# Optimization experiments

Hardware: AMD Instinct MI355X
Metric: run time of the kernel (lower is better)

Reference implementation:

```python
import jax, jax.numpy as jnp
import numpy as np

EMBED_DIM = 2048
NUM_HEADS = 16
NUM_GROUPS = 4
HEAD_DIM = EMBED_DIM // NUM_HEADS  # 128
B, S = 2, 2048


def setup_inputs() -> dict:
    key = jax.random.key(0)
    ks = jax.random.split(key, 7)
    sc = 0.02
    return {
        "x": jax.random.normal(ks[0], (B, S, EMBED_DIM), dtype=jnp.float32),
        "Wq": jax.random.normal(ks[1], (EMBED_DIM, EMBED_DIM), dtype=jnp.float32) * sc,
        "bq": jnp.zeros((EMBED_DIM,), dtype=jnp.float32),
        "Wkv": jax.random.normal(ks[2], (EMBED_DIM, 2 * EMBED_DIM // NUM_GROUPS), dtype=jnp.float32) * sc,
        "bkv": jnp.zeros((2 * EMBED_DIM // NUM_GROUPS,), dtype=jnp.float32),
        "Wo": jax.random.normal(ks[3], (EMBED_DIM, EMBED_DIM), dtype=jnp.float32) * sc,
        "bo": jnp.zeros((EMBED_DIM,), dtype=jnp.float32),
    }


def reference(x, Wq, bq, Wkv, bkv, Wo, bo):
    b, s, e = x.shape
    group_size = NUM_HEADS // NUM_GROUPS
    # projections (torch Linear: x @ W + b with W stored [in, out] here)
    q = (x @ Wq + bq).reshape(b, s, NUM_HEADS, HEAD_DIM).transpose(0, 2, 1, 3)   # [B,H,S,D]
    kv = (x @ Wkv + bkv).reshape(b, s, NUM_GROUPS, 2 * HEAD_DIM).transpose(0, 2, 1, 3)  # [B,G,S,2D]
    k, v = kv[..., :HEAD_DIM], kv[..., HEAD_DIM:]                                # [B,G,S,D]
    # repeat each kv group for its heads (matches repeat_interleave on head dim)
    k = jnp.repeat(k, group_size, axis=1)                                        # [B,H,S,D]
    v = jnp.repeat(v, group_size, axis=1)                                        # [B,H,S,D]
    scores = jnp.einsum("bhqd,bhkd->bhqk", q, k) / (HEAD_DIM ** 0.5)             # [B,H,S,S]
    attn = jax.nn.softmax(scores, axis=-1)
    out = jnp.einsum("bhqk,bhkd->bhqd", attn, v)                                 # [B,H,S,D]
    out = out.transpose(0, 2, 1, 3).reshape(b, s, e)
    return out @ Wo + bo
```

## Files before the change

kernel.cpp:

```cpp
#include <hip/hip_runtime.h>

#define DEV __device__ __forceinline__

typedef unsigned short u16;
typedef unsigned int u32;
using bf16x8 = __attribute__((ext_vector_type(8))) __bf16;
using f32x4v = __attribute__((ext_vector_type(4))) float;

typedef __attribute__((address_space(1))) void gas_void;
typedef __attribute__((address_space(3))) void las_void;

DEV u16 f32_bf16(float f){
  u32 u = __float_as_uint(f);
  u += 0x7FFFu + ((u >> 16) & 1u);
  return (u16)(u >> 16);
}
DEV float bf16_f32(u16 h){ return __uint_as_float(((u32)h) << 16); }

DEV void gload16(const void* g, void* l){
  __builtin_amdgcn_global_load_lds((gas_void*)g, (las_void*)l, 16, 0, 0);
}

DEV float exp2_hw(float x){
  float r;
  asm("v_exp_f32 %0, %1" : "=v"(r) : "v"(x));
  return r;
}

#define QSCL 0.12752333f

__global__ void cvt_f32_bf16_k(const float* __restrict__ in, u16* __restrict__ out, int n){
  int i = (blockIdx.x * 256 + threadIdx.x) * 8;
  if (i >= n) return;
  float4 a = *(const float4*)(in + i);
  float4 b = *(const float4*)(in + i + 4);
  uint4 r;
  r.x = (u32)f32_bf16(a.x) | ((u32)f32_bf16(a.y) << 16);
  r.y = (u32)f32_bf16(a.z) | ((u32)f32_bf16(a.w) << 16);
  r.z = (u32)f32_bf16(b.x) | ((u32)f32_bf16(b.y) << 16);
  r.w = (u32)f32_bf16(b.z) | ((u32)f32_bf16(b.w) << 16);
  *(uint4*)(out + i) = r;
}

template<typename T>
__global__ void transpose_cvt_k(const T* __restrict__ in, u16* __restrict__ out, int R, int C){
  in  += (size_t)blockIdx.z * R * C;
  out += (size_t)blockIdx.z * R * C;
  __shared__ float tile[64][65];
  int c0 = blockIdx.x * 64, r0 = blockIdx.y * 64;
  int t = threadIdx.x;
  int lr = t >> 4;
  int lc = (t & 15) * 4;
  #pragma unroll
  for (int p = 0; p < 4; p++){
    int row = p * 16 + lr;
    const T* src = in + (size_t)(r0 + row) * C + c0 + lc;
    float v0, v1, v2, v3;
    if constexpr (sizeof(T) == 4){
      float4 v = *(const float4*)src;
      v0 = v.x; v1 = v.y; v2 = v.z; v3 = v.w;
    } else {
      ushort4 v = *(const ushort4*)src;
      v0 = bf16_f32(v.x); v1 = bf16_f32(v.y); v2 = bf16_f32(v.z); v3 = bf16_f32(v.w);
    }
    tile[row][lc+0] = v0; tile[row][lc+1] = v1; tile[row][lc+2] = v2; tile[row][lc+3] = v3;
  }
  __syncthreads();
  #pragma unroll
  for (int p = 0; p < 4; p++){
    int ocol = p * 16 + lr;
    ushort4 w;
    w.x = f32_bf16(tile[lc+0][ocol]);
    w.y = f32_bf16(tile[lc+1][ocol]);
    w.z = f32_bf16(tile[lc+2][ocol]);
    w.w = f32_bf16(tile[lc+3][ocol]);
    *(ushort4*)(out + (size_t)(c0 + ocol) * R + r0 + lc) = w;
  }
}

__global__ __launch_bounds__(512, 2)
void gemm256_k(const u16* __restrict__ A, const u16* __restrict__ BT,
               const float* __restrict__ bias0, const float* __restrict__ bias1,
               u16* __restrict__ outQ, u16* __restrict__ outK, u16* __restrict__ outV,
               float* __restrict__ outF, int K, int mode)
{
  __shared__ __align__(16) u16 sA[4][256*32];
  __shared__ __align__(16) u16 sB[4][256*32];
  const int t = threadIdx.x;
  const int l = t & 63, wv = t >> 6;
  const int wm = wv >> 2, wn = wv & 3;
  const int rl = l & 15, gr = l >> 4;
  const size_t m0 = (size_t)blockIdx.x * 256, n0 = (size_t)blockIdx.y * 256;
  const u16* gA = A + m0 * K;
  const u16* gB = BT + n0 * K;

  const u16* gAs[2]; const u16* gBs[2]; int ldso[2];
  #pragma unroll
  for (int j = 0; j < 2; j++){
    int c = t + j * 512;
    int row = c >> 2, cl = c & 3;
    int clp = cl ^ ((row >> 1) & 3);
    gAs[j] = gA + (size_t)row * K + clp * 8;
    gBs[j] = gB + (size_t)row * K + clp * 8;
    ldso[j] = c * 8;
  }
  auto stage = [&](int kt){
    int buf = kt & 3;
    int k0 = kt * 32;
    #pragma unroll
    for (int j = 0; j < 2; j++){
      gload16(gAs[j] + k0, &sA[buf][ldso[j]]);
      gload16(gBs[j] + k0, &sB[buf][ldso[j]]);
    }
  };

  const int swz8 = (gr ^ ((rl >> 1) & 3)) * 8;
  int offA[8], offB[4];
  #pragma unroll
  for (int mr = 0; mr < 8; mr++) offA[mr] = (wm*128 + mr*16 + rl) * 32 + swz8;
  #pragma unroll
  for (int nr = 0; nr < 4; nr++) offB[nr] = (wn*64 + nr*16 + rl) * 32 + swz8;

  f32x4v acc[8][4];
  #pragma unroll
  for (int i = 0; i < 8; i++)
    #pragma unroll
    for (int j = 0; j < 4; j++)
      acc[i][j] = (f32x4v)(0.0f);

  const int NT = K / 32;
  stage(0); stage(1);
  asm volatile("s_waitcnt vmcnt(4)" ::: "memory");
  __builtin_amdgcn_s_barrier();

  for (int kt = 0; kt < NT; kt++){
    const u16* sa = sA[kt & 3];
    const u16* sb = sB[kt & 3];
    bf16x8 af[8], bfr[4];
    #pragma unroll
    for (int mr = 0; mr < 8; mr++) af[mr] = *(const bf16x8*)(sa + offA[mr]);
    #pragma unroll
    for (int nr = 0; nr < 4; nr++) bfr[nr] = *(const bf16x8*)(sb + offB[nr]);
    if (kt + 2 < NT){
      stage(kt + 2);
      asm volatile("s_waitcnt vmcnt(4)" ::: "memory");
    } else {
      asm volatile("s_waitcnt vmcnt(0)" ::: "memory");
    }
    __builtin_amdgcn_s_barrier();
    __builtin_amdgcn_s_setprio(1);
    #pragma unroll
    for (int mr = 0; mr < 8; mr++)
      #pragma unroll
      for (int nr = 0; nr < 4; nr++)
        acc[mr][nr] = __builtin_amdgcn_mfma_f32_16x16x32_bf16(af[mr], bfr[nr], acc[mr][nr], 0, 0, 0);
    __builtin_amdgcn_s_setprio(0);
  }

  #pragma unroll
  for (int nr = 0; nr < 4; nr++){
    int col = (int)n0 + wn*64 + nr*16 + rl;
    float bv = (mode == 2 || col < 2048) ? bias0[col < 2048 ? col : 0] : 0.0f;
    if (mode != 2 && col >= 2048) bv = bias1[col - 2048];
    #pragma unroll
    for (int mr = 0; mr < 8; mr++){
      int rowb = (int)m0 + wm*128 + mr*16 + gr*4;
      #pragma unroll
      for (int r = 0; r < 4; r++){
        int row = rowb + r;
        float v = acc[mr][nr][r] + bv;
        if (mode == 2){
          outF[(size_t)row * 2048 + col] = v;
        } else if (col < 2048){
          int b = row >> 11, s = row & 2047, h = col >> 7, d = col & 127;
          outQ[(((size_t)(b*16 + h)) * 2048 + s) * 128 + d] = f32_bf16(v * QSCL);
        } else {
          int b = row >> 11, s = row & 2047;
          int c2 = col - 2048, g = c2 >> 8, cc = c2 & 255;
          u16* dst = (cc < 128) ? outK : outV;
          dst[(((size_t)(b*4 + g)) * 2048 + s) * 128 + (cc & 127)] = f32_bf16(v);
        }
      }
    }
  }
}

__global__ __launch_bounds__(256, 2)
void attn_k(const u16* __restrict__ Q, const u16* __restrict__ Kb,
            const u16* __restrict__ VT, u16* __restrict__ O)
{
  __shared__ __align__(16) u16 sK[2][64*128];
  __shared__ __align__(16) u16 sV[2][128*64];
  __shared__ __align__(16) u16 Plds[4][16*72];
  const int t = threadIdx.x, l = t & 63, wv = t >> 6;
  const int rl = l & 15, gr = l >> 4;
  const int bh = blockIdx.y;
  const int b = bh >> 4, h = bh & 15, g = h >> 2;
  const int q0 = blockIdx.x * 64 + wv * 16;
  const u16* Qp = Q + ((size_t)(b*16 + h) * 2048 + q0) * 128;
  const u16* Kp = Kb + (size_t)(b*4 + g) * 2048 * 128;
  const u16* Vp = VT + (size_t)(b*4 + g) * 128 * 2048;

  bf16x8 qf[4];
  #pragma unroll
  for (int ds = 0; ds < 4; ds++)
    qf[ds] = *(const bf16x8*)(Qp + rl*128 + ds*32 + gr*8);

  f32x4v acc_o[8];
  #pragma unroll
  for (int i = 0; i < 8; i++) acc_o[i] = (f32x4v)(0.0f);
  float m_run = -3.0e38f, l_run = 0.0f;

  auto stageKV = [&](int buf, int kt){
    const int kv0 = kt * 64;
    const u16* Ksrc = Kp + (size_t)kv0 * 128;
    #pragma unroll
    for (int j = 0; j < 4; j++){
      int n16 = j * 256 + t;
      int row = n16 >> 4, cl = n16 & 15;
      int sc = cl ^ (row & 7);
      gload16(Ksrc + row * 128 + sc * 8, &sK[buf][n16 * 8]);
    }
    const u16* Vsrc = Vp + kv0;
    #pragma unroll
    for (int j = 0; j < 4; j++){
      int n16 = j * 256 + t;
      int row = n16 >> 3, cl = n16 & 7;
      int sc = cl ^ (row & 7);
      gload16(Vsrc + (size_t)row * 2048 + sc * 8, &sV[buf][n16 * 8]);
    }
  };

  stageKV(0, 0);
  asm volatile("s_waitcnt vmcnt(0)" ::: "memory");
  __syncthreads();

  for (int kt = 0; kt < 32; kt++){
    const int cur = kt & 1;
    if (kt + 1 < 32) stageKV(cur ^ 1, kt + 1);
    const u16* sk = sK[cur];
    const u16* sv = sV[cur];

    float pv[4][4];
    float tm = -3.0e38f;
    #pragma unroll
    for (int tt = 0; tt < 4; tt++){
      f32x4v st = (f32x4v)(0.0f);
      bf16x8 kf[4];
      #pragma unroll
      for (int ds = 0; ds < 4; ds++){
        int r = tt*16 + rl;
        int c = ds*4 + gr;
        kf[ds] = *(const bf16x8*)(sk + r*128 + ((c ^ (r & 7)) * 8));
      }
      __builtin_amdgcn_s_setprio(1);
      #pragma unroll
      for (int ds = 0; ds < 4; ds++)
        st = __builtin_amdgcn_mfma_f32_16x16x32_bf16(kf[ds], qf[ds], st, 0, 0, 0);
      __builtin_amdgcn_s_setprio(0);
      #pragma unroll
      for (int r = 0; r < 4; r++){
        pv[tt][r] = st[r];
        tm = fmaxf(tm, st[r]);
      }
    }
    tm = fmaxf(tm, __shfl_xor(tm, 16, 64));
    tm = fmaxf(tm, __shfl_xor(tm, 32, 64));
    if (!__all(tm <= m_run + 11.0f)){
      float m_new = fmaxf(m_run, tm);
      float corr = exp2_hw(m_run - m_new);
      l_run *= corr;
      float cr0 = __shfl(corr, gr*4 + 0, 64);
      float cr1 = __shfl(corr, gr*4 + 1, 64);
      float cr2 = __shfl(corr, gr*4 + 2, 64);
      float cr3 = __shfl(corr, gr*4 + 3, 64);
      #pragma unroll
      for (int dc = 0; dc < 8; dc++){
        acc_o[dc][0] *= cr0; acc_o[dc][1] *= cr1; acc_o[dc][2] *= cr2; acc_o[dc][3] *= cr3;
      }
      m_run = m_new;
    }
    float psum = 0.f;
    #pragma unroll
    for (int tt = 0; tt < 4; tt++)
      #pragma unroll
      for (int r = 0; r < 4; r++){
        float p = exp2_hw(pv[tt][r] - m_run);
        pv[tt][r] = p;
        psum += p;
      }
    psum += __shfl_xor(psum, 16, 64);
    psum += __shfl_xor(psum, 32, 64);
    l_run += psum;

    #pragma unroll
    for (int tt = 0; tt < 4; tt++){
      ushort4 pk;
      pk.x = f32_bf16(pv[tt][0]); pk.y = f32_bf16(pv[tt][1]);
      pk.z = f32_bf16(pv[tt][2]); pk.w = f32_bf16(pv[tt][3]);
      *(ushort4*)&Plds[wv][rl*72 + tt*16 + gr*4] = pk;
    }
    asm volatile("s_waitcnt lgkmcnt(0)" ::: "memory");
    #pragma unroll
    for (int kc = 0; kc < 2; kc++){
      bf16x8 pa = *(const bf16x8*)&Plds[wv][rl*72 + kc*32 + gr*8];
      bf16x8 vf[8];
      #pragma unroll
      for (int dc = 0; dc < 8; dc++){
        int r = dc*16 + rl;
        int c = kc*4 + gr;
        vf[dc] = *(const bf16x8*)(sv + r*64 + ((c ^ (r & 7)) * 8));
      }
      __builtin_amdgcn_s_setprio(1);
      #pragma unroll
      for (int dc = 0; dc < 8; dc++)
        acc_o[dc] = __builtin_amdgcn_mfma_f32_16x16x32_bf16(pa, vf[dc], acc_o[dc], 0, 0, 0);
      __builtin_amdgcn_s_setprio(0);
    }
    asm volatile("s_waitcnt vmcnt(0)" ::: "memory");
    __syncthreads();
  }
  float linv = 1.0f / l_run;
  float lr0 = __shfl(linv, gr*4 + 0, 64);
  float lr1 = __shfl(linv, gr*4 + 1, 64);
  float lr2 = __shfl(linv, gr*4 + 2, 64);
  float lr3 = __shfl(linv, gr*4 + 3, 64);
  float lrr[4] = {lr0, lr1, lr2, lr3};
  #pragma unroll
  for (int dc = 0; dc < 8; dc++)
    #pragma unroll
    for (int r = 0; r < 4; r++){
      size_t idx = ((size_t)b * 2048 + q0 + gr*4 + r) * 2048 + h*128 + dc*16 + rl;
      O[idx] = f32_bf16(acc_o[dc][r] * lrr[r]);
    }
}

extern "C" void kernel_launch(void* const* d_in, const int* in_sizes, int n_in,
                              void* d_out, int out_size, void* d_ws, size_t ws_size,
                              hipStream_t stream)
{
  const float* x   = (const float*)d_in[0];
  const float* Wq  = (const float*)d_in[1];
  const float* bq  = (const float*)d_in[2];
  const float* Wkv = (const float*)d_in[3];
  const float* bkv = (const float*)d_in[4];
  const float* Wo  = (const float*)d_in[5];
  const float* bo  = (const float*)d_in[6];
  float* out = (float*)d_out;

  char* ws = (char*)d_ws;
  size_t off = 0;
  auto alloc = [&](size_t bytes){ void* p = ws + off; off = (off + bytes + 255) & ~(size_t)255; return p; };
  u16* xb     = (u16*)alloc(8388608ull * 2);
  u16* WqkvT  = (u16*)alloc(6291456ull * 2);
  u16* WoT    = (u16*)alloc(4194304ull * 2);
  u16* Qb     = (u16*)alloc(8388608ull * 2);
  u16* Kb     = (u16*)alloc(2097152ull * 2);
  u16* Vb     = (u16*)alloc(2097152ull * 2);
  u16* VTb    = (u16*)alloc(2097152ull * 2);
  u16* Ob     = (u16*)alloc(8388608ull * 2);

  cvt_f32_bf16_k<<<4096, 256, 0, stream>>>(x, xb, 8388608);
  transpose_cvt_k<float><<<dim3(32, 32, 1), 256, 0, stream>>>(Wq,  WqkvT, 2048, 2048);
  transpose_cvt_k<float><<<dim3(16, 32, 1), 256, 0, stream>>>(Wkv, WqkvT + 2048ull*2048ull, 2048, 1024);
  transpose_cvt_k<float><<<dim3(32, 32, 1), 256, 0, stream>>>(Wo,  WoT, 2048, 2048);

  gemm256_k<<<dim3(16, 12), 512, 0, stream>>>(xb, WqkvT, bq, bkv, Qb, Kb, Vb, nullptr, 2048, 0);

  transpose_cvt_k<u16><<<dim3(2, 32, 8), 256, 0, stream>>>(Vb, VTb, 2048, 128);

  attn_k<<<dim3(32, 32), 256, 0, stream>>>(Qb, Kb, VTb, Ob);

  gemm256_k<<<dim3(16, 8), 512, 0, stream>>>(Ob, WoT, bo, nullptr, nullptr, nullptr, nullptr, out, 2048, 2);
}
```

Baseline: 354.2 us.

## Use 32x32 MFMA attention with register P, fuse V transpose, narrow output GEMM

The attention kernel moves from 16x16x32 to 32x32x16 MFMA with 32 query rows per wave and 128 per block. The softmax probabilities are repacked in registers via cvt_pk and a lane-swap shuffle instead of a round trip through LDS. The QKV GEMM epilogue now writes V already transposed, which removes the separate transpose kernel and the Vb buffer. The output projection gets its own 256x128-tile GEMM so it launches 256 blocks instead of 128 for better CU fill. The trade-off is higher register pressure in attention and half as many attention blocks (512 instead of 1024).

```diff
diff --git a/kernel.cpp b/kernel.cpp
--- a/kernel.cpp
+++ b/kernel.cpp
@@ -6,6 +6,7 @@
 typedef unsigned int u32;
 using bf16x8 = __attribute__((ext_vector_type(8))) __bf16;
 using f32x4v = __attribute__((ext_vector_type(4))) float;
+using f32x16 = __attribute__((ext_vector_type(16))) float;
 
 typedef __attribute__((address_space(1))) void gas_void;
 typedef __attribute__((address_space(3))) void las_void;
@@ -25,6 +26,16 @@
   float r;
   asm("v_exp_f32 %0, %1" : "=v"(r) : "v"(x));
   return r;
+}
+DEV u32 cvtpk_bf16(float lo, float hi){
+  u32 r;
+  asm("v_cvt_pk_bf16_f32 %0, %1, %2" : "=v"(r) : "v"(lo), "v"(hi));
+  return r;
+}
+DEV bf16x8 mk_bf16x8(u32 a, u32 b, u32 c, u32 d){
+  union { u32 w[4]; bf16x8 v; } u;
+  u.w[0] = a; u.w[1] = b; u.w[2] = c; u.w[3] = d;
+  return u.v;
 }
 
 #define QSCL 0.12752333f
@@ -81,8 +92,8 @@
 __global__ __launch_bounds__(512, 2)
 void gemm256_k(const u16* __restrict__ A, const u16* __restrict__ BT,
                const float* __restrict__ bias0, const float* __restrict__ bias1,
-               u16* __restrict__ outQ, u16* __restrict__ outK, u16* __restrict__ outV,
-               float* __restrict__ outF, int K, int mode)
+               u16* __restrict__ outQ, u16* __restrict__ outK, u16* __restrict__ outVT,
+               int K)
 {
   __shared__ __align__(16) u16 sA[4][256*32];
   __shared__ __align__(16) u16 sB[4][256*32];
@@ -160,27 +171,127 @@
   #pragma unroll
   for (int nr = 0; nr < 4; nr++){
     int col = (int)n0 + wn*64 + nr*16 + rl;
-    float bv = (mode == 2 || col < 2048) ? bias0[col < 2048 ? col : 0] : 0.0f;
-    if (mode != 2 && col >= 2048) bv = bias1[col - 2048];
+    float bv = (col < 2048) ? bias0[col] : bias1[col - 2048];
     #pragma unroll
     for (int mr = 0; mr < 8; mr++){
       int rowb = (int)m0 + wm*128 + mr*16 + gr*4;
-      #pragma unroll
-      for (int r = 0; r < 4; r++){
-        int row = rowb + r;
-        float v = acc[mr][nr][r] + bv;
-        if (mode == 2){
-          outF[(size_t)row * 2048 + col] = v;
-        } else if (col < 2048){
-          int b = row >> 11, s = row & 2047, h = col >> 7, d = col & 127;
-          outQ[(((size_t)(b*16 + h)) * 2048 + s) * 128 + d] = f32_bf16(v * QSCL);
+      int b = rowb >> 11, s0 = rowb & 2047;
+      if (col < 2048){
+        int h = col >> 7, d = col & 127;
+        #pragma unroll
+        for (int r = 0; r < 4; r++)
+          outQ[(((size_t)(b*16 + h)) * 2048 + s0 + r) * 128 + d] =
+            f32_bf16((acc[mr][nr][r] + bv) * QSCL);
+      } else {
+        int c2 = col - 2048, g = c2 >> 8, cc = c2 & 255;
+        if (cc < 128){
+          #pragma unroll
+          for (int r = 0; r < 4; r++)
+            outK[(((size_t)(b*4 + g)) * 2048 + s0 + r) * 128 + cc] =
+              f32_bf16(acc[mr][nr][r] + bv);
         } else {
-          int b = row >> 11, s = row & 2047;
-          int c2 = col - 2048, g = c2 >> 8, cc = c2 & 255;
-          u16* dst = (cc < 128) ? outK : outV;
-          dst[(((size_t)(b*4 + g)) * 2048 + s) * 128 + (cc & 127)] = f32_bf16(v);
+          int d = cc - 128;
+          ushort4 w;
+          w.x = f32_bf16(acc[mr][nr][0] + bv);
+          w.y = f32_bf16(acc[mr][nr][1] + bv);
+          w.z = f32_bf16(acc[mr][nr][2] + bv);
+          w.w = f32_bf16(acc[mr][nr][3] + bv);
+          *(ushort4*)&outVT[(((size_t)(b*4 + g)) * 128 + d) * 2048 + s0] = w;
         }
       }
+    }
+  }
+}
+
+__global__ __launch_bounds__(512, 2)
+void gemm_o_k(const u16* __restrict__ A, const u16* __restrict__ BT,
+              const float* __restrict__ bias, float* __restrict__ outF, int K)
+{
+  __shared__ __align__(16) u16 sA[4][256*32];
+  __shared__ __align__(16) u16 sB[4][128*32];
+  const int t = threadIdx.x;
+  const int l = t & 63, wv = t >> 6;
+  const int wm = wv >> 2, wn = wv & 3;
+  const int rl = l & 15, gr = l >> 4;
+  const size_t m0 = (size_t)blockIdx.x * 256, n0 = (size_t)blockIdx.y * 128;
+  const u16* gA = A + m0 * K;
+  const u16* gB = BT + n0 * K;
+
+  const u16* gAs[2]; int ldsoA[2];
+  #pragma unroll
+  for (int j = 0; j < 2; j++){
+    int c = t + j * 512;
+    int row = c >> 2, cl = c & 3;
+    int clp = cl ^ ((row >> 1) & 3);
+    gAs[j] = gA + (size_t)row * K + clp * 8;
+    ldsoA[j] = c * 8;
+  }
+  const int rowB = t >> 2;
+  const int clB = (t & 3) ^ ((rowB >> 1) & 3);
+  const u16* gBs = gB + (size_t)rowB * K + clB * 8;
+  const int ldsoB = t * 8;
+
+  auto stage = [&](int kt){
+    int buf = kt & 3;
+    int k0 = kt * 32;
+    gload16(gAs[0] + k0, &sA[buf][ldsoA[0]]);
+    gload16(gAs[1] + k0, &sA[buf][ldsoA[1]]);
+    gload16(gBs + k0, &sB[buf][ldsoB]);
+  };
+
+  const int swz8 = (gr ^ ((rl >> 1) & 3)) * 8;
+  int offA[8], offB[2];
+  #pragma unroll
+  for (int mr = 0; mr < 8; mr++) offA[mr] = (wm*128 + mr*16 + rl) * 32 + swz8;
+  #pragma unroll
+  for (int nr = 0; nr < 2; nr++) offB[nr] = (wn*32 + nr*16 + rl) * 32 + swz8;
+
+  f32x4v acc[8][2];
+  #pragma unroll
+  for (int i = 0; i < 8; i++)
+    #pragma unroll
+    for (int j = 0; j < 2; j++)
+      acc[i][j] = (f32x4v)(0.0f);
+
+  const int NT = K / 32;
+  stage(0); stage(1);
+  asm volatile("s_waitcnt vmcnt(3)" ::: "memory");
+  __builtin_amdgcn_s_barrier();
+
+  for (int kt = 0; kt < NT; kt++){
+    const u16* sa = sA[kt & 3];
+    const u16* sb = sB[kt & 3];
+    bf16x8 af[8], bfr[2];
+    #pragma unroll
+    for (int mr = 0; mr < 8; mr++) af[mr] = *(const bf16x8*)(sa + offA[mr]);
+    #pragma unroll
+    for (int nr = 0; nr < 2; nr++) bfr[nr] = *(const bf16x8*)(sb + offB[nr]);
+    if (kt + 2 < NT){
+      stage(kt + 2);
+      asm volatile("s_waitcnt vmcnt(3)" ::: "memory");
+    } else {
+      asm volatile("s_waitcnt vmcnt(0)" ::: "memory");
+    }
+    __builtin_amdgcn_s_barrier();
+    __builtin_amdgcn_s_setprio(1);
+    #pragma unroll
+    for (int mr = 0; mr < 8; mr++)
+      #pragma unroll
+      for (int nr = 0; nr < 2; nr++)
+        acc[mr][nr] = __builtin_amdgcn_mfma_f32_16x16x32_bf16(af[mr], bfr[nr], acc[mr][nr], 0, 0, 0);
+    __builtin_amdgcn_s_setprio(0);
+  }
+
+  #pragma unroll
+  for (int nr = 0; nr < 2; nr++){
+    int col = (int)n0 + wn*32 + nr*16 + rl;
+    float bv = bias[col];
+    #pragma unroll
+    for (int mr = 0; mr < 8; mr++){
+      int rowb = (int)m0 + wm*128 + mr*16 + gr*4;
+      #pragma unroll
+      for (int r = 0; r < 4; r++)
+        outF[(size_t)(rowb + r) * 2048 + col] = acc[mr][nr][r] + bv;
     }
   }
 }
@@ -191,24 +302,23 @@
 {
   __shared__ __align__(16) u16 sK[2][64*128];
   __shared__ __align__(16) u16 sV[2][128*64];
-  __shared__ __align__(16) u16 Plds[4][16*72];
   const int t = threadIdx.x, l = t & 63, wv = t >> 6;
-  const int rl = l & 15, gr = l >> 4;
+  const int lq = l & 31, hi = l >> 5;
   const int bh = blockIdx.y;
   const int b = bh >> 4, h = bh & 15, g = h >> 2;
-  const int q0 = blockIdx.x * 64 + wv * 16;
+  const int q0 = blockIdx.x * 128 + wv * 32;
   const u16* Qp = Q + ((size_t)(b*16 + h) * 2048 + q0) * 128;
   const u16* Kp = Kb + (size_t)(b*4 + g) * 2048 * 128;
   const u16* Vp = VT + (size_t)(b*4 + g) * 128 * 2048;
 
-  bf16x8 qf[4];
-  #pragma unroll
-  for (int ds = 0; ds < 4; ds++)
-    qf[ds] = *(const bf16x8*)(Qp + rl*128 + ds*32 + gr*8);
-
-  f32x4v acc_o[8];
-  #pragma unroll
-  for (int i = 0; i < 8; i++) acc_o[i] = (f32x4v)(0.0f);
+  bf16x8 qf[8];
+  #pragma unroll
+  for (int ds = 0; ds < 8; ds++)
+    qf[ds] = *(const bf16x8*)(Qp + (size_t)lq*128 + ds*16 + hi*8);
+
+  f32x16 acc[4];
+  #pragma unroll
+  for (int i = 0; i < 4; i++) acc[i] = (f32x16)(0.0f);
   float m_run = -3.0e38f, l_run = 0.0f;
 
   auto stageKV = [&](int buf, int kt){
@@ -241,98 +351,96 @@
     const u16* sk = sK[cur];
     const u16* sv = sV[cur];
 
-    float pv[4][4];
+    f32x16 p[2];
+    #pragma unroll
+    for (int kt2 = 0; kt2 < 2; kt2++){
+      f32x16 st = (f32x16)(0.0f);
+      const int row = kt2*32 + lq;
+      const u16* skr = sk + row*128;
+      const int rx = row & 7;
+      __builtin_amdgcn_s_setprio(1);
+      #pragma unroll
+      for (int ds = 0; ds < 8; ds++){
+        bf16x8 kf = *(const bf16x8*)(skr + (((ds*2 + hi) ^ rx) * 8));
+        st = __builtin_amdgcn_mfma_f32_32x32x16_bf16(kf, qf[ds], st, 0, 0, 0);
+      }
+      __builtin_amdgcn_s_setprio(0);
+      p[kt2] = st;
+    }
+
     float tm = -3.0e38f;
     #pragma unroll
-    for (int tt = 0; tt < 4; tt++){
-      f32x4v st = (f32x4v)(0.0f);
-      bf16x8 kf[4];
-      #pragma unroll
-      for (int ds = 0; ds < 4; ds++){
-        int r = tt*16 + rl;
-        int c = ds*4 + gr;
-        kf[ds] = *(const bf16x8*)(sk + r*128 + ((c ^ (r & 7)) * 8));
-      }
-      __builtin_amdgcn_s_setprio(1);
-      #pragma unroll
-      for (int ds = 0; ds < 4; ds++)
-        st = __builtin_amdgcn_mfma_f32_16x16x32_bf16(kf[ds], qf[ds], st, 0, 0, 0);
-      __builtin_amdgcn_s_setprio(0);
-      #pragma unroll
-      for (int r = 0; r < 4; r++){
-        pv[tt][r] = st[r];
-        tm = fmaxf(tm, st[r]);
-      }
-    }
-    tm = fmaxf(tm, __shfl_xor(tm, 16, 64));
+    for (int r = 0; r < 16; r++) tm = fmaxf(tm, fmaxf(p[0][r], p[1][r]));
     tm = fmaxf(tm, __shfl_xor(tm, 32, 64));
     if (!__all(tm <= m_run + 11.0f)){
       float m_new = fmaxf(m_run, tm);
       float corr = exp2_hw(m_run - m_new);
       l_run *= corr;
-      float cr0 = __shfl(corr, gr*4 + 0, 64);
-      float cr1 = __shfl(corr, gr*4 + 1, 64);
-      float cr2 = __shfl(corr, gr*4 + 2, 64);
-      float cr3 = __shfl(corr, gr*4 + 3, 64);
-      #pragma unroll
-      for (int dc = 0; dc < 8; dc++){
-        acc_o[dc][0] *= cr0; acc_o[dc][1] *= cr1; acc_o[dc][2] *= cr2; acc_o[dc][3] *= cr3;
+      #pragma unroll
+      for (int r = 0; r < 16; r++){
+        float cr = __shfl(corr, (r&3) + 8*(r>>2) + 4*hi, 64);
+        acc[0][r] *= cr; acc[1][r] *= cr; acc[2][r] *= cr; acc[3][r] *= cr;
       }
       m_run = m_new;
     }
-    float psum = 0.f;
-    #pragma unroll
-    for (int tt = 0; tt < 4; tt++)
-      #pragma unroll
-      for (int r = 0; r < 4; r++){
-        float p = exp2_hw(pv[tt][r] - m_run);
-        pv[tt][r] = p;
-        psum += p;
-      }
-    psum += __shfl_xor(psum, 16, 64);
-    psum += __shfl_xor(psum, 32, 64);
-    l_run += psum;
-
-    #pragma unroll
-    for (int tt = 0; tt < 4; tt++){
-      ushort4 pk;
-      pk.x = f32_bf16(pv[tt][0]); pk.y = f32_bf16(pv[tt][1]);
-      pk.z = f32_bf16(pv[tt][2]); pk.w = f32_bf16(pv[tt][3]);
-      *(ushort4*)&Plds[wv][rl*72 + tt*16 + gr*4] = pk;
-    }
-    asm volatile("s_waitcnt lgkmcnt(0)" ::: "memory");
-    #pragma unroll
-    for (int kc = 0; kc < 2; kc++){
-      bf16x8 pa = *(const bf16x8*)&Plds[wv][rl*72 + kc*32 + gr*8];
-      bf16x8 vf[8];
-      #pragma unroll
-      for (int dc = 0; dc < 8; dc++){
-        int r = dc*16 + rl;
-        int c = kc*4 + gr;
-        vf[dc] = *(const bf16x8*)(sv + r*64 + ((c ^ (r & 7)) * 8));
-      }
+    float ps = 0.0f;
+    #pragma unroll
+    for (int kt2 = 0; kt2 < 2; kt2++)
+      #pragma unroll
+      for (int r = 0; r < 16; r++){
+        float v = exp2_hw(p[kt2][r] - m_run);
+        p[kt2][r] = v; ps += v;
+      }
+    ps += __shfl_xor(ps, 32, 64);
+    l_run += ps;
+
+    bf16x8 pa[4];
+    #pragma unroll
+    for (int kt2 = 0; kt2 < 2; kt2++){
+      #pragma unroll
+      for (int ks2 = 0; ks2 < 2; ks2++){
+        u32 X  = cvtpk_bf16(p[kt2][8*ks2+0], p[kt2][8*ks2+1]);
+        u32 X2 = cvtpk_bf16(p[kt2][8*ks2+2], p[kt2][8*ks2+3]);
+        u32 Y  = cvtpk_bf16(p[kt2][8*ks2+4], p[kt2][8*ks2+5]);
+        u32 Y2 = cvtpk_bf16(p[kt2][8*ks2+6], p[kt2][8*ks2+7]);
+        u32 Xo  = (u32)__shfl_xor((int)X,  32, 64);
+        u32 X2o = (u32)__shfl_xor((int)X2, 32, 64);
+        u32 Yo  = (u32)__shfl_xor((int)Y,  32, 64);
+        u32 Y2o = (u32)__shfl_xor((int)Y2, 32, 64);
+        u32 W0 = hi ? Yo  : X;
+        u32 W1 = hi ? Y2o : X2;
+        u32 W2 = hi ? Y   : Xo;
+        u32 W3 = hi ? Y2  : X2o;
+        pa[kt2*2 + ks2] = mk_bf16x8(W0, W1, W2, W3);
+      }
+    }
+
+    #pragma unroll
+    for (int ks = 0; ks < 4; ks++){
       __builtin_amdgcn_s_setprio(1);
       #pragma unroll
-      for (int dc = 0; dc < 8; dc++)
-        acc_o[dc] = __builtin_amdgcn_mfma_f32_16x16x32_bf16(pa, vf[dc], acc_o[dc], 0, 0, 0);
+      for (int dt = 0; dt < 4; dt++){
+        const int row = dt*32 + lq;
+        bf16x8 vf = *(const bf16x8*)(sv + row*64 + ((((ks<<1) + hi) ^ (row & 7)) * 8));
+        acc[dt] = __builtin_amdgcn_mfma_f32_32x32x16_bf16(pa[ks], vf, acc[dt], 0, 0, 0);
+      }
       __builtin_amdgcn_s_setprio(0);
     }
+
     asm volatile("s_waitcnt vmcnt(0)" ::: "memory");
     __syncthreads();
   }
+
   float linv = 1.0f / l_run;
-  float lr0 = __shfl(linv, gr*4 + 0, 64);
-  float lr1 = __shfl(linv, gr*4 + 1, 64);
-  float lr2 = __shfl(linv, gr*4 + 2, 64);
-  float lr3 = __shfl(linv, gr*4 + 3, 64);
-  float lrr[4] = {lr0, lr1, lr2, lr3};
-  #pragma unroll
-  for (int dc = 0; dc < 8; dc++)
-    #pragma unroll
-    for (int r = 0; r < 4; r++){
-      size_t idx = ((size_t)b * 2048 + q0 + gr*4 + r) * 2048 + h*128 + dc*16 + rl;
-      O[idx] = f32_bf16(acc_o[dc][r] * lrr[r]);
-    }
+  #pragma unroll
+  for (int r = 0; r < 16; r++){
+    int qq = (r&3) + 8*(r>>2) + 4*hi;
+    float li = __shfl(linv, qq, 64);
+    size_t rowo = ((size_t)b * 2048 + q0 + qq) * 2048 + h*128 + lq;
+    #pragma unroll
+    for (int dt = 0; dt < 4; dt++)
+      O[rowo + dt*32] = f32_bf16(acc[dt][r] * li);
+  }
 }
 
 extern "C" void kernel_launch(void* const* d_in, const int* in_sizes, int n_in,
@@ -356,7 +464,6 @@
   u16* WoT    = (u16*)alloc(4194304ull * 2);
   u16* Qb     = (u16*)alloc(8388608ull * 2);
   u16* Kb     = (u16*)alloc(2097152ull * 2);
-  u16* Vb     = (u16*)alloc(2097152ull * 2);
   u16* VTb    = (u16*)alloc(2097152ull * 2);
   u16* Ob     = (u16*)alloc(8388608ull * 2);
 
@@ -365,11 +472,9 @@
   transpose_cvt_k<float><<<dim3(16, 32, 1), 256, 0, stream>>>(Wkv, WqkvT + 2048ull*2048ull, 2048, 1024);
   transpose_cvt_k<float><<<dim3(32, 32, 1), 256, 0, stream>>>(Wo,  WoT, 2048, 2048);
 
-  gemm256_k<<<dim3(16, 12), 512, 0, stream>>>(xb, WqkvT, bq, bkv, Qb, Kb, Vb, nullptr, 2048, 0);
-
-  transpose_cvt_k<u16><<<dim3(2, 32, 8), 256, 0, stream>>>(Vb, VTb, 2048, 128);
-
-  attn_k<<<dim3(32, 32), 256, 0, stream>>>(Qb, Kb, VTb, Ob);
-
-  gemm256_k<<<dim3(16, 8), 512, 0, stream>>>(Ob, WoT, bo, nullptr, nullptr, nullptr, nullptr, out, 2048, 2);
-}
+  gemm256_k<<<dim3(16, 12), 512, 0, stream>>>(xb, WqkvT, bq, bkv, Qb, Kb, VTb, 2048);
+
+  attn_k<<<dim3(16, 32), 256, 0, stream>>>(Qb, Kb, VTb, Ob);
+
+  gemm_o_k<<<dim3(16, 16), 512, 0, stream>>>(Ob, WoT, bo, out, 2048);
+}
```

Measured after the change: 314.8 us. 11.1% less time.
